# Kernel tuning notes

Hardware: AMD Instinct MI355X
Metric: run time of the kernel (lower is better)

The kernel has to match this reference:

```python
import jax, jax.numpy as jnp
import numpy as np

# Model constants (from Equilibrium3BConfig + hardcoded MambaBlock args)
D_MODEL = 2560
D_INNER = 5120          # expand=2
N_STATE = 128           # d_state
HEADS = 80              # d_inner // headdim
P_HEAD = 64             # headdim
D_CONV = 4
CONV_DIM = D_INNER + 2 * N_STATE        # 5376 (x, B, C share the conv)
D_IN_PROJ = 2 * D_INNER + 2 * N_STATE + HEADS  # 10576 (z, xBC, dt)
N_EXPERTS = 16
TOP_K = 2
M_INTER = 864
MS_INTER = 1728
EPS = 1e-6


def _rms(x, w, eps=EPS):
    xf = x.astype(jnp.float32)
    xf = xf * jax.lax.rsqrt(jnp.mean(xf * xf, axis=-1, keepdims=True) + eps)
    return w * xf.astype(x.dtype)


def setup_inputs() -> dict:
    key = jax.random.key(0)
    ks = jax.random.split(key, 16)
    b, l = 1, 1024
    s = 0.02  # weight scale, keeps activations sane through the deep block
    return {
        "hidden_states": jax.random.normal(ks[0], (b, l, D_MODEL), jnp.float32),
        "w_in": jax.random.normal(ks[1], (D_MODEL, D_IN_PROJ), jnp.float32) * s,
        "conv_w": jax.random.normal(ks[2], (CONV_DIM, D_CONV), jnp.float32) * s,
        "conv_b": jnp.zeros((CONV_DIM,), jnp.float32),
        "dt_bias": jax.random.normal(ks[3], (HEADS,), jnp.float32) * s,
        "A_log": jax.random.normal(ks[4], (HEADS,), jnp.float32) * s,
        "D": jnp.ones((HEADS,), jnp.float32),
        "mamba_norm_w": jnp.ones((D_INNER,), jnp.float32),
        "w_out": jax.random.normal(ks[5], (D_INNER, D_MODEL), jnp.float32) * s,
        "ln1_w": jnp.ones((D_MODEL,), jnp.float32),
        "ln2_w": jnp.ones((D_MODEL,), jnp.float32),
        "router_w": jax.random.normal(ks[6], (D_MODEL, N_EXPERTS), jnp.float32) * s,
        "we_gate": jax.random.normal(ks[7], (N_EXPERTS, D_MODEL, M_INTER), jnp.float32) * s,
        "we_up": jax.random.normal(ks[8], (N_EXPERTS, D_MODEL, M_INTER), jnp.float32) * s,
        "we_down": jax.random.normal(ks[9], (N_EXPERTS, M_INTER, D_MODEL), jnp.float32) * s,
        "ws_gate": jax.random.normal(ks[10], (D_MODEL, MS_INTER), jnp.float32) * s,
        "ws_up": jax.random.normal(ks[11], (D_MODEL, MS_INTER), jnp.float32) * s,
        "ws_down": jax.random.normal(ks[12], (MS_INTER, D_MODEL), jnp.float32) * s,
    }


def _forward(hidden_states, w_in, conv_w, conv_b, dt_bias, A_log, D, mamba_norm_w,
             w_out, ln1_w, ln2_w, router_w, we_gate, we_up, we_down,
             ws_gate, ws_up, ws_down):
    b, l, d = hidden_states.shape

    # ---- Mamba2 (selective scan) sub-block ----
    residual = hidden_states
    x = _rms(hidden_states, ln1_w)
    zxbcdt = x @ w_in  # [b, l, 10576]
    z, xBC, dt = jnp.split(zxbcdt, [D_INNER, D_INNER + CONV_DIM], axis=-1)

    # depthwise causal conv over (x, B, C) channels, then SiLU
    xBC_t = xBC.transpose(0, 2, 1)  # [b, c, l]
    conv = jax.lax.conv_general_dilated(
        xBC_t, conv_w[:, None, :], (1,), [(D_CONV - 1, 0)],
        feature_group_count=CONV_DIM, dimension_numbers=("NCH", "OIH", "NCH"))
    xBC = jax.nn.silu((conv + conv_b[None, :, None]).transpose(0, 2, 1))
    xs, Bc, Cc = jnp.split(xBC, [D_INNER, D_INNER + N_STATE], axis=-1)

    dt = jax.nn.softplus(dt + dt_bias)          # [b, l, h]
    A = -jnp.exp(A_log)                          # [h]
    xh = xs.reshape(b, l, HEADS, P_HEAD)

    # time-major for scan
    dt_l = dt.transpose(1, 0, 2)                 # [l, b, h]
    xh_l = xh.transpose(1, 0, 2, 3)              # [l, b, h, p]
    B_l = Bc.transpose(1, 0, 2)                  # [l, b, n]
    C_l = Cc.transpose(1, 0, 2)                  # [l, b, n]

    def step(h, inp):
        dt_t, x_t, B_t, C_t = inp
        dA = jnp.exp(dt_t * A)                   # [b, h]
        h = h * dA[..., None, None] + (dt_t[..., None] * x_t)[..., None] * B_t[:, None, None, :]
        y = jnp.einsum("bhpn,bn->bhp", h, C_t)
        return h, y

    h0 = jnp.zeros((b, HEADS, P_HEAD, N_STATE), hidden_states.dtype)
    _, y_l = jax.lax.scan(step, h0, (dt_l, xh_l, B_l, C_l))
    y_l = y_l + D[None, None, :, None] * xh_l    # skip term
    y = y_l.transpose(1, 0, 2, 3).reshape(b, l, D_INNER)
    y = _rms(y * jax.nn.silu(z), mamba_norm_w)   # gated RMSNorm
    hidden = residual + y @ w_out

    # ---- DeepSeekMoE sub-block ----
    residual2 = hidden
    xm = _rms(hidden, ln2_w).reshape(b * l, d)
    logits = xm @ router_w
    probs = jax.nn.softmax(logits.astype(jnp.float32), axis=-1)
    topv, topi = jax.lax.top_k(probs, TOP_K)
    topv = topv / jnp.sum(topv, axis=-1, keepdims=True)  # renormalize top-k
    wdense = jnp.sum(jax.nn.one_hot(topi, N_EXPERTS, dtype=xm.dtype)
                     * topv[..., None].astype(xm.dtype), axis=1)  # [T, E]

    # routed experts (SwiGLU), dense-masked faithful math
    hexp = (jax.nn.silu(jnp.einsum("td,edm->tem", xm, we_gate))
            * jnp.einsum("td,edm->tem", xm, we_up))
    y_routed = jnp.einsum("tem,emd,te->td", hexp, we_down, wdense)

    # shared experts (single fused SwiGLU MLP)
    y_shared = (jax.nn.silu(xm @ ws_gate) * (xm @ ws_up)) @ ws_down

    moe = (y_routed + y_shared).reshape(b, l, d)
    return residual2 + moe


def reference(hidden_states, w_in, conv_w, conv_b, dt_bias, A_log, D, mamba_norm_w,
              w_out, ln1_w, ln2_w, router_w, we_gate, we_up, we_down,
              ws_gate, ws_up, ws_down):
    return _forward(hidden_states, w_in, conv_w, conv_b, dt_bias, A_log, D,
                    mamba_norm_w, w_out, ln1_w, ln2_w, router_w,
                    we_gate, we_up, we_down, ws_gate, ws_up, ws_down)
```

## Files before the change

### kernel.cpp

```cpp
#include <hip/hip_runtime.h>

typedef __attribute__((ext_vector_type(4))) float f32x4;
typedef __attribute__((ext_vector_type(8))) __bf16 bf16x8;
typedef __attribute__((ext_vector_type(4))) __bf16 bf16x4;
typedef __attribute__((ext_vector_type(8))) _Float16 f16x8;
typedef __attribute__((ext_vector_type(4))) _Float16 f16x4;

#define D_MODEL 2560
#define D_INNER 5120
#define N_STATE 128
#define HEADS 80
#define P_HEAD 64
#define CONV_DIM 5376
#define D_INPROJ 10576
#define SEQ 1024
#define NCHUNK 16
#define QCHUNK 64
#define NEXP 16
#define M_INTER 864
#define MS_INTER 1728
#define NSLOT 2048
#define NSLOTP 2176

__device__ __forceinline__ float siluf(float x) { return x / (1.f + __expf(-x)); }

__device__ __forceinline__ int swz_p(int k4, int P) {
  return (k4 & ~31) | ((((k4 >> 3) & 3) ^ P) << 3) | (k4 & 7);
}
__device__ __forceinline__ int swz64(int k4, int row) {
  return (k4 & ~63) | (((((k4 >> 3) & 7) ^ (row & 7)) << 3)) | (k4 & 7);
}

__device__ __forceinline__ void gl16(const __bf16* g, __bf16* l) {
  __builtin_amdgcn_global_load_lds((const __attribute__((address_space(1))) unsigned int*)g,
                                   (__attribute__((address_space(3))) unsigned int*)l, 16, 0, 0);
}

__device__ __forceinline__ float block_sum256(float v, float* red) {
#pragma unroll
  for (int m = 32; m > 0; m >>= 1) v += __shfl_xor(v, m, 64);
  int w = threadIdx.x >> 6;
  if ((threadIdx.x & 63) == 0) red[w] = v;
  __syncthreads();
  return red[0] + red[1] + red[2] + red[3];
}

template <bool FP16>
__global__ __launch_bounds__(256) void k_rmsnorm_p(const float* __restrict__ in,
                                                   const float* __restrict__ w,
                                                   float* __restrict__ f32out,
                                                   __bf16* __restrict__ ph,
                                                   __bf16* __restrict__ pdh,
                                                   __bf16* __restrict__ pdl, int D) {
  __shared__ float red[4];
  int t = blockIdx.x, tid = threadIdx.x;
  const float* x = in + (size_t)t * D;
  int nd4 = D >> 2;
  float ss = 0.f;
  for (int i = tid; i < nd4; i += 256) {
    float4 v = ((const float4*)x)[i];
    ss += v.x * v.x + v.y * v.y + v.z * v.z + v.w * v.w;
  }
  float tot = block_sum256(ss, red);
  float r = rsqrtf(tot / (float)D + 1e-6f);
  int P = (t >> 1) & 3;
  for (int i = tid; i < nd4; i += 256) {
    float4 v = ((const float4*)x)[i];
    float4 wv = ((const float4*)w)[i];
    float4 o;
    o.x = wv.x * v.x * r; o.y = wv.y * v.y * r; o.z = wv.z * v.z * r; o.w = wv.w * v.w * r;
    if (f32out) ((float4*)(f32out + (size_t)t * D))[i] = o;
    int p64 = swz64(i * 4, t);
    if constexpr (FP16) {
      f16x4 hv;
      hv[0] = (_Float16)o.x; hv[1] = (_Float16)o.y; hv[2] = (_Float16)o.z; hv[3] = (_Float16)o.w;
      *(f16x4*)&ph[(size_t)t * D + p64] = hv;
    } else {
      bf16x4 hv;
      hv[0] = (__bf16)o.x; hv[1] = (__bf16)o.y; hv[2] = (__bf16)o.z; hv[3] = (__bf16)o.w;
      *(bf16x4*)&ph[(size_t)t * D + p64] = hv;
    }
    if (pdh) {
      int p = swz_p(i * 4, P);
      bf16x4 hv, lv;
      hv[0] = (__bf16)o.x; hv[1] = (__bf16)o.y; hv[2] = (__bf16)o.z; hv[3] = (__bf16)o.w;
      lv[0] = (__bf16)(o.x - (float)hv[0]); lv[1] = (__bf16)(o.y - (float)hv[1]);
      lv[2] = (__bf16)(o.z - (float)hv[2]); lv[3] = (__bf16)(o.w - (float)hv[3]);
      *(bf16x4*)&pdh[(size_t)t * D + p] = hv;
      *(bf16x4*)&pdl[(size_t)t * D + p] = lv;
    }
  }
}

template <bool SPLIT, bool FP16>
__global__ __launch_bounds__(256) void k_transW(const float* __restrict__ W, int ld, int K, int N,
                                                __bf16* __restrict__ Th, __bf16* __restrict__ Tl) {
  __shared__ float T[64][65];
  const int n0 = blockIdx.x * 64, k0 = blockIdx.y * 64, tid = threadIdx.x;
#pragma unroll
  for (int i = 0; i < 16; i++) {
    int idx = tid + i * 256;
    int k = idx >> 6, n = idx & 63;
    float v = 0.f;
    if (n0 + n < N) v = W[(size_t)(k0 + k) * ld + n0 + n];
    T[k][n] = v;
  }
  __syncthreads();
#pragma unroll
  for (int i = 0; i < 4; i++) {
    int idx = tid + i * 256;
    int n = idx >> 4, p4 = (idx & 15) * 4;
    int nn = n0 + n;
    if constexpr (SPLIT) {
      int P = (nn >> 1) & 3;
      bf16x4 hv, lv;
#pragma unroll
      for (int e = 0; e < 4; e++) {
        int p = p4 + e;
        int kk = (p & ~31) | ((((p >> 3) & 3) ^ P) << 3) | (p & 7);
        float v = T[kk][n];
        __bf16 h = (__bf16)v;
        hv[e] = h;
        lv[e] = (__bf16)(v - (float)h);
      }
      *(bf16x4*)&Th[(size_t)nn * K + k0 + p4] = hv;
      *(bf16x4*)&Tl[(size_t)nn * K + k0 + p4] = lv;
    } else if constexpr (FP16) {
      f16x4 hv;
#pragma unroll
      for (int e = 0; e < 4; e++) {
        int p = p4 + e;
        int kk = swz64(p, nn);
        hv[e] = (_Float16)T[kk][n];
      }
      *(f16x4*)&Th[(size_t)nn * K + k0 + p4] = hv;
    } else {
      bf16x4 hv;
#pragma unroll
      for (int e = 0; e < 4; e++) {
        int p = p4 + e;
        int kk = swz64(p, nn);
        hv[e] = (__bf16)T[kk][n];
      }
      *(bf16x4*)&Th[(size_t)nn * K + k0 + p4] = hv;
    }
  }
}

template <bool SPLIT, bool FP16, int BK, bool PIPE>
__global__ __launch_bounds__(256) void k_gemm2(const __bf16* __restrict__ Ah,
                                               const __bf16* __restrict__ Al,
                                               const __bf16* __restrict__ Bh,
                                               const __bf16* __restrict__ Bl,
                                               float* __restrict__ C,
                                               int M, int N, int K, int ks, int nst) {
  constexpr int PLE = 128 * BK;
  constexpr int NPL = SPLIT ? 4 : 2;
  constexpr int NBUF = PIPE ? 2 : 1;
  constexpr int CALLS = PLE / 2048;
  constexpr int CPR = BK / 8;
  constexpr int RPC = 256 / CPR;
  constexpr int KSUB = BK / 32;
  __shared__ __bf16 lds[NBUF * NPL * PLE];

  const int tid = threadIdx.x;
  const int T = gridDim.x * gridDim.y * gridDim.z;
  const int linear = blockIdx.x + gridDim.x * (blockIdx.y + gridDim.y * blockIdx.z);
  const int s_idx = (linear & 7) * (T >> 3) + (linear >> 3);
  const int bm = s_idx & 7;
  const int g = s_idx >> 3;
  const int bn = g % gridDim.y;
  const int z = g / gridDim.y;

  const int m0 = bm * 128, n0 = bn * 128;
  const int s0 = (int)(((long long)z * nst) / ks);
  const int s1 = (int)(((long long)(z + 1) * nst) / ks);
  float* __restrict__ Cp = C + (size_t)z * M * N;

  const int lane = tid & 63, wid = tid >> 6;
  const int wr = wid >> 1, wc = wid & 1;
  const int l16 = lane & 15, kl = lane >> 4;

  const int srow = tid / CPR;
  const int schunk = (tid % CPR) * 8;
  size_t aB[CALLS], bB[CALLS];
#pragma unroll
  for (int i = 0; i < CALLS; i++) {
    aB[i] = (size_t)(m0 + srow + RPC * i) * K + schunk;
    bB[i] = (size_t)(n0 + srow + RPC * i) * K + schunk;
  }

  int aoff[4][KSUB], boff[4][KSUB];
#pragma unroll
  for (int mi = 0; mi < 4; mi++) {
    int ra = wr * 64 + mi * 16 + l16;
    int rb = wc * 64 + mi * 16 + l16;
#pragma unroll
    for (int kk = 0; kk < KSUB; kk++) {
      if constexpr (BK == 32) {
        aoff[mi][kk] = ra * 64 + ((kl ^ ((ra >> 1) & 3)) << 4);
        boff[mi][kk] = rb * 64 + ((kl ^ ((rb >> 1) & 3)) << 4);
      } else {
        aoff[mi][kk] = ra * (2 * BK) + (((kk * 4 + kl) ^ (ra & 7)) << 4);
        boff[mi][kk] = rb * (2 * BK) + (((kk * 4 + kl) ^ (rb & 7)) << 4);
      }
    }
  }

  f32x4 acc[4][4];
#pragma unroll
  for (int mi = 0; mi < 4; mi++)
#pragma unroll
    for (int ni = 0; ni < 4; ni++) acc[mi][ni] = f32x4{0.f, 0.f, 0.f, 0.f};

  auto STAGE = [&](int b, int kof) {
    __bf16* L = lds + (size_t)b * NPL * PLE;
#pragma unroll
    for (int i = 0; i < CALLS; i++) {
      gl16(Ah + aB[i] + kof, L + (tid + i * 256) * 8);
      gl16(Bh + bB[i] + kof, L + (SPLIT ? 2 : 1) * PLE + (tid + i * 256) * 8);
      if constexpr (SPLIT) {
        gl16(Al + aB[i] + kof, L + PLE + (tid + i * 256) * 8);
        gl16(Bl + bB[i] + kof, L + 3 * PLE + (tid + i * 256) * 8);
      }
    }
  };

  auto COMPUTE = [&](const __bf16* L) {
    const char* AsH = (const char*)L;
    const char* BsH = (const char*)(L + (SPLIT ? 2 : 1) * PLE);
#pragma unroll
    for (int kk = 0; kk < KSUB; kk++) {
      if constexpr (!SPLIT && FP16) {
        f16x8 ah[4], bh[4];
#pragma unroll
        for (int mi = 0; mi < 4; mi++) ah[mi] = *(const f16x8*)(AsH + aoff[mi][kk]);
#pragma unroll
        for (int ni = 0; ni < 4; ni++) bh[ni] = *(const f16x8*)(BsH + boff[ni][kk]);
#pragma unroll
        for (int mi = 0; mi < 4; mi++)
#pragma unroll
          for (int ni = 0; ni < 4; ni++)
            acc[mi][ni] = __builtin_amdgcn_mfma_f32_16x16x32_f16(ah[mi], bh[ni], acc[mi][ni], 0, 0, 0);
      } else {
        bf16x8 ah[4], bh[4];
#pragma unroll
        for (int mi = 0; mi < 4; mi++) ah[mi] = *(const bf16x8*)(AsH + aoff[mi][kk]);
#pragma unroll
        for (int ni = 0; ni < 4; ni++) bh[ni] = *(const bf16x8*)(BsH + boff[ni][kk]);
#pragma unroll
        for (int mi = 0; mi < 4; mi++)
#pragma unroll
          for (int ni = 0; ni < 4; ni++)
            acc[mi][ni] = __builtin_amdgcn_mfma_f32_16x16x32_bf16(ah[mi], bh[ni], acc[mi][ni], 0, 0, 0);
        if constexpr (SPLIT) {
          const char* AsL = (const char*)(L + PLE);
          const char* BsL = (const char*)(L + 3 * PLE);
          bf16x8 al[4], bl[4];
#pragma unroll
          for (int mi = 0; mi < 4; mi++) al[mi] = *(const bf16x8*)(AsL + aoff[mi][kk]);
#pragma unroll
          for (int ni = 0; ni < 4; ni++) bl[ni] = *(const bf16x8*)(BsL + boff[ni][kk]);
#pragma unroll
          for (int mi = 0; mi < 4; mi++)
#pragma unroll
            for (int ni = 0; ni < 4; ni++) {
              acc[mi][ni] = __builtin_amdgcn_mfma_f32_16x16x32_bf16(ah[mi], bl[ni], acc[mi][ni], 0, 0, 0);
              acc[mi][ni] = __builtin_amdgcn_mfma_f32_16x16x32_bf16(al[mi], bh[ni], acc[mi][ni], 0, 0, 0);
            }
        }
      }
    }
  };

  if constexpr (PIPE) {
    STAGE(0, s0 * BK);
    __syncthreads();
    int cur = 0;
    for (int s = s0; s < s1; ++s) {
      if (s + 1 < s1) STAGE(cur ^ 1, (s + 1) * BK);
      COMPUTE(lds + (size_t)cur * NPL * PLE);
      __syncthreads();
      cur ^= 1;
    }
  } else {
    for (int s = s0; s < s1; ++s) {
      __syncthreads();
      STAGE(0, s * BK);
      __syncthreads();
      COMPUTE(lds);
    }
  }

#pragma unroll
  for (int mi = 0; mi < 4; mi++)
#pragma unroll
    for (int ni = 0; ni < 4; ni++)
#pragma unroll
      for (int r = 0; r < 4; r++) {
        int row = m0 + wr * 64 + mi * 16 + kl * 4 + r;
        int col = n0 + wc * 64 + ni * 16 + l16;
        if (col < N) Cp[(size_t)row * N + col] = acc[mi][ni][r];
      }
}

template <bool RES>
__global__ void k_reduce(const float* __restrict__ Pp, int np, int n4,
                         const float* __restrict__ res, float* __restrict__ out) {
  int i = blockIdx.x * 256 + threadIdx.x;
  int stride = gridDim.x * 256;
  for (; i < n4; i += stride) {
    float4 a = ((const float4*)Pp)[i];
    for (int z = 1; z < np; z++) {
      float4 b = ((const float4*)Pp)[(size_t)z * n4 + i];
      a.x += b.x; a.y += b.y; a.z += b.z; a.w += b.w;
    }
    if constexpr (RES) {
      float4 r0 = ((const float4*)res)[i];
      a.x += r0.x; a.y += r0.y; a.z += r0.z; a.w += r0.w;
    }
    ((float4*)out)[i] = a;
  }
}

__global__ void k_dtfin(const float* __restrict__ dtP, const float* __restrict__ dt_bias,
                        const float* __restrict__ A_log, float* __restrict__ dtp,
                        float* __restrict__ dtA) {
  int t = blockIdx.x, h = threadIdx.x;
  if (h < HEADS) {
    float v = dt_bias[h];
#pragma unroll
    for (int z = 0; z < 8; z++) v += dtP[((size_t)z * SEQ + t) * 80 + h];
    float sp = fmaxf(v, 0.f) + log1pf(expf(-fabsf(v)));
    dtp[t * HEADS + h] = sp;
    dtA[t * HEADS + h] = sp * (-expf(A_log[h]));
  }
}

__global__ __launch_bounds__(256) void k_gatherA(const float* __restrict__ xm,
                                                 const int* __restrict__ perm,
                                                 __bf16* __restrict__ Aslots) {
  int s = blockIdx.x, tid = threadIdx.x;
  int t = perm[s];
  int P = (s >> 1) & 3;
  const float* src = xm + (size_t)t * D_MODEL;
  __bf16* dst = Aslots + (size_t)s * D_MODEL;
  for (int i = tid; i < D_MODEL / 4; i += 256) {
    float4 v = ((const float4*)src)[i];
    int p = swz_p(i * 4, P);
    bf16x4 h;
    h[0] = (__bf16)v.x; h[1] = (__bf16)v.y; h[2] = (__bf16)v.z; h[3] = (__bf16)v.w;
    *(bf16x4*)&dst[p] = h;
  }
}

template <int KS>
__global__ __launch_bounds__(256) void k_gemmE2(const __bf16* __restrict__ Aall,
                                                const float* __restrict__ Bg,
                                                float* __restrict__ Cp,
                                                const int* __restrict__ expOff,
                                                const int* __restrict__ expCnt,
                                                int N, int K, long long strideB) {
  __shared__ __bf16 Asl[2][128 * 32];
  __shared__ __bf16 Bsl[2][128][40];
  const int tid = threadIdx.x;
  const int bn = blockIdx.x, ks = blockIdx.y, e = blockIdx.z;
  const int cnt = expCnt[e], base = expOff[e];
  if (cnt == 0) return;
  const float* Bp = Bg + (long long)e * strideB;
  const int n0 = bn * 128;
  const int kChunk = K / KS, kBeg = ks * kChunk, nIter = kChunk / 32;
  float* __restrict__ Cpl = Cp + (size_t)ks * NSLOTP * N;
  const int lane = tid & 63, wid = tid >> 6;
  const int wr = wid >> 1, wc = wid & 1;
  const int l16 = lane & 15, kl = lane >> 4;
  const int kb = tid >> 5, cb = tid & 31;
  const int arow = tid >> 2, achk = (tid & 3) * 8;
  const bool bok = (n0 + cb * 4) < N;

  int boffs[4];
#pragma unroll
  for (int ni = 0; ni < 4; ni++) boffs[ni] = (wc * 64 + ni * 16 + l16) * 40 + kl * 8;

  for (int bm = 0; bm * 128 < cnt; ++bm) {
    const int rbase = base + bm * 128;
    int aoff[4];
#pragma unroll
    for (int mi = 0; mi < 4; mi++) {
      int r = wr * 64 + mi * 16 + l16;
      int P = ((rbase + r) >> 1) & 3;
      aoff[mi] = r * 64 + ((kl ^ P) << 4);
    }
    f32x4 acc[4][4];
#pragma unroll
    for (int mi = 0; mi < 4; mi++)
#pragma unroll
      for (int ni = 0; ni < 4; ni++) acc[mi][ni] = f32x4{0.f, 0.f, 0.f, 0.f};

    const size_t aBase = (size_t)(rbase + arow) * K + achk + kBeg;
    const size_t aBase2 = aBase + (size_t)64 * K;

    gl16(Aall + aBase, &Asl[0][tid * 8]);
    gl16(Aall + aBase2, &Asl[0][(tid + 256) * 8]);
    {
      const float* src = Bp + (size_t)(kBeg + kb * 4) * N + n0 + cb * 4;
      f32x4 bv[4];
#pragma unroll
      for (int j = 0; j < 4; j++)
        bv[j] = bok ? *(const f32x4*)(src + (size_t)j * N) : f32x4{0.f, 0.f, 0.f, 0.f};
#pragma unroll
      for (int e4 = 0; e4 < 4; e4++) {
        bf16x4 h;
        h[0] = (__bf16)bv[0][e4]; h[1] = (__bf16)bv[1][e4];
        h[2] = (__bf16)bv[2][e4]; h[3] = (__bf16)bv[3][e4];
        *(bf16x4*)&Bsl[0][cb * 4 + e4][kb * 4] = h;
      }
    }
    __syncthreads();
    int cur = 0;
    for (int kt = 0; kt < nIter; ++kt) {
      const bool more = (kt + 1 < nIter);
      f32x4 nv[4];
      if (more) {
        const int kOff = (kt + 1) * 32;
        gl16(Aall + aBase + kOff, &Asl[cur ^ 1][tid * 8]);
// ... 16 lines not shown
      if (more) {
#pragma unroll
        for (int e4 = 0; e4 < 4; e4++) {
          bf16x4 h;
          h[0] = (__bf16)nv[0][e4]; h[1] = (__bf16)nv[1][e4];
          h[2] = (__bf16)nv[2][e4]; h[3] = (__bf16)nv[3][e4];
          *(bf16x4*)&Bsl[cur ^ 1][cb * 4 + e4][kb * 4] = h;
        }
      }
      __syncthreads();
      cur ^= 1;
    }
#pragma unroll
    for (int mi = 0; mi < 4; mi++)
#pragma unroll
      for (int ni = 0; ni < 4; ni++)
#pragma unroll
        for (int r = 0; r < 4; r++) {
          int rl = bm * 128 + wr * 64 + mi * 16 + kl * 4 + r;
          int col = n0 + wc * 64 + ni * 16 + l16;
          if (rl < cnt && col < N) Cpl[(size_t)(base + rl) * N + col] = acc[mi][ni][r];
        }
  }
}

__global__ __launch_bounds__(256) void k_silumulE(const float* __restrict__ gP,
                                                  const float* __restrict__ uP,
                                                  const float* __restrict__ slotw,
                                                  __bf16* __restrict__ outp) {
  int s = blockIdx.x, tid = threadIdx.x;
  float w = slotw[s];
  int P = (s >> 1) & 3;
  const size_t PL = (size_t)NSLOTP * M_INTER;
  for (int i = tid; i < M_INTER / 4; i += 256) {
    f32x4 g = f32x4{0.f, 0.f, 0.f, 0.f}, u = f32x4{0.f, 0.f, 0.f, 0.f};
#pragma unroll
    for (int z = 0; z < 4; z++) {
      g += *(const f32x4*)&gP[z * PL + (size_t)s * M_INTER + i * 4];
      u += *(const f32x4*)&uP[z * PL + (size_t)s * M_INTER + i * 4];
    }
    int p = swz_p(i * 4, P);
    bf16x4 h;
    h[0] = (__bf16)(siluf(g[0]) * u[0] * w);
    h[1] = (__bf16)(siluf(g[1]) * u[1] * w);
    h[2] = (__bf16)(siluf(g[2]) * u[2] * w);
    h[3] = (__bf16)(siluf(g[3]) * u[3] * w);
    *(bf16x4*)&outp[(size_t)s * M_INTER + p] = h;
  }
}

__global__ __launch_bounds__(256) void k_silumul_sh2(const float* __restrict__ P4,
                                                     __bf16* __restrict__ outp) {
  int t = blockIdx.x, tid = threadIdx.x;
  const size_t PL = (size_t)SEQ * 3456;
  for (int i = tid; i < MS_INTER / 4; i += 256) {
    f32x4 g = f32x4{0.f, 0.f, 0.f, 0.f}, u = f32x4{0.f, 0.f, 0.f, 0.f};
#pragma unroll
    for (int z = 0; z < 4; z++) {
      g += *(const f32x4*)&P4[z * PL + (size_t)t * 3456 + i * 4];
      u += *(const f32x4*)&P4[z * PL + (size_t)t * 3456 + 1728 + i * 4];
    }
    int p = swz64(i * 4, t);
    bf16x4 h;
    h[0] = (__bf16)(siluf(g[0]) * u[0]);
    h[1] = (__bf16)(siluf(g[1]) * u[1]);
    h[2] = (__bf16)(siluf(g[2]) * u[2]);
    h[3] = (__bf16)(siluf(g[3]) * u[3]);
    *(bf16x4*)&outp[(size_t)t * MS_INTER + p] = h;
  }
}

__global__ void k_conv(const float* __restrict__ zx, const float* __restrict__ cw,
                       const float* __restrict__ cb, float* __restrict__ xBC) {
  int cidx = blockIdx.x * 256 + threadIdx.x;
  int t = blockIdx.y;
  if (cidx < CONV_DIM) {
    float acc = cb[cidx];
#pragma unroll
    for (int j = 0; j < 4; j++) {
      int tt = t - 3 + j;
      if (tt >= 0) acc += zx[(size_t)tt * D_INPROJ + D_INNER + cidx] * cw[cidx * 4 + j];
    }
    xBC[(size_t)t * CONV_DIM + cidx] = siluf(acc);
  }
}

__global__ __launch_bounds__(256) void k_scan_intra(
    const float* __restrict__ xBC, const float* __restrict__ dtp,
    const float* __restrict__ dtA, float* __restrict__ y, float* __restrict__ S,
    float* __restrict__ cumA, float* __restrict__ Atot) {
  __shared__ float Bs[64 * 128];
  __shared__ float CG[64 * 128];
  __shared__ _Float16 Xs[64 * 64];
  __shared__ float da_s[64], a_s[64], dt_sh[64], w_sh[64];
  int c = blockIdx.x, h = blockIdx.y, tid = threadIdx.x;
  int t0 = c * QCHUNK;
#pragma unroll
  for (int i = 0; i < 8; i++) {
    int id = tid + 256 * i;
    int r = id >> 5, nc = id & 31;
    int sc = (nc ^ ((r >> 2) & 7)) * 4;
    *(float4*)&Bs[r * 128 + sc] = *(const float4*)&xBC[(size_t)(t0 + r) * CONV_DIM + D_INNER + nc * 4];
    *(float4*)&CG[r * 128 + sc] = *(const float4*)&xBC[(size_t)(t0 + r) * CONV_DIM + D_INNER + N_STATE + nc * 4];
  }
#pragma unroll
  for (int i = 0; i < 4; i++) {
    int id = tid + 256 * i;
    int r = id >> 4, p4 = (id & 15) * 4;
    float4 v = *(const float4*)&xBC[(size_t)(t0 + r) * CONV_DIM + h * P_HEAD + p4];
    f16x4 hv;
    hv[0] = (_Float16)v.x; hv[1] = (_Float16)v.y; hv[2] = (_Float16)v.z; hv[3] = (_Float16)v.w;
    *(f16x4*)&Xs[r * 64 + p4] = hv;
  }
  if (tid < 64) {
    da_s[tid] = dtA[(size_t)(t0 + tid) * HEADS + h];
// ... 133 lines not shown
#pragma unroll
  for (int j = 0; j < 4; j++) acc[j] = float4{0.f, 0.f, 0.f, 0.f};
  for (int nc = 0; nc < 32; nc++) {
    float4 cv[4], hv[4];
#pragma unroll
    for (int j = 0; j < 4; j++) {
      int rt = tq * 4 + j;
      cv[j] = *(const float4*)&Cs[rt * 128 + ((nc ^ ((rt >> 2) & 7)) * 4)];
      int rp = pq * 4 + j;
      hv[j] = *(const float4*)&Hs[rp * 128 + ((nc ^ ((rp >> 2) & 7)) * 4)];
    }
#pragma unroll
    for (int j = 0; j < 4; j++) {
      acc[j].x += cv[j].x * hv[0].x + cv[j].y * hv[0].y + cv[j].z * hv[0].z + cv[j].w * hv[0].w;
      acc[j].y += cv[j].x * hv[1].x + cv[j].y * hv[1].y + cv[j].z * hv[1].z + cv[j].w * hv[1].w;
      acc[j].z += cv[j].x * hv[2].x + cv[j].y * hv[2].y + cv[j].z * hv[2].z + cv[j].w * hv[2].w;
      acc[j].w += cv[j].x * hv[3].x + cv[j].y * hv[3].y + cv[j].z * hv[3].z + cv[j].w * hv[3].w;
    }
  }
#pragma unroll
  for (int j = 0; j < 4; j++) {
    int t = tq * 4 + j;
    float e = __expf(a_l[t]);
    float4 xv = *(const float4*)&xBC[(size_t)(t0 + t) * CONV_DIM + h * P_HEAD + pq * 4];
    size_t yoff = (size_t)(t0 + t) * D_INNER + h * P_HEAD + pq * 4;
    float4 yv = *(float4*)&y[yoff];
    yv.x += e * acc[j].x + Dh * xv.x;
    yv.y += e * acc[j].y + Dh * xv.y;
    yv.z += e * acc[j].z + Dh * xv.z;
    yv.w += e * acc[j].w + Dh * xv.w;
    *(float4*)&y[yoff] = yv;
  }
}

__global__ __launch_bounds__(256) void k_gatednorm_p(const float* __restrict__ y,
                                                     const float* __restrict__ zx,
                                                     const float* __restrict__ w,
                                                     __bf16* __restrict__ ph) {
  __shared__ float vbuf[D_INNER];
  __shared__ float red[4];
  int t = blockIdx.x, tid = threadIdx.x;
  float ss = 0.f;
  for (int i = tid; i < D_INNER / 4; i += 256) {
    float4 yv = *(const float4*)&y[(size_t)t * D_INNER + i * 4];
    float4 zv = *(const float4*)&zx[(size_t)t * D_INPROJ + i * 4];
    float4 v;
    v.x = yv.x * siluf(zv.x); v.y = yv.y * siluf(zv.y);
    v.z = yv.z * siluf(zv.z); v.w = yv.w * siluf(zv.w);
    *(float4*)&vbuf[i * 4] = v;
    ss += v.x * v.x + v.y * v.y + v.z * v.z + v.w * v.w;
  }
  float tot = block_sum256(ss, red);
  float r = rsqrtf(tot / (float)D_INNER + 1e-6f);
  for (int i = tid; i < D_INNER / 4; i += 256) {
    float4 v = *(const float4*)&vbuf[i * 4];
    float4 wv = *(const float4*)&w[i * 4];
    float4 o;
    o.x = wv.x * v.x * r; o.y = wv.y * v.y * r; o.z = wv.z * v.z * r; o.w = wv.w * v.w * r;
    int p = swz64(i * 4, t);
    f16x4 hv;
    hv[0] = (_Float16)o.x; hv[1] = (_Float16)o.y; hv[2] = (_Float16)o.z; hv[3] = (_Float16)o.w;
    *(f16x4*)&ph[(size_t)t * D_INNER + p] = hv;
  }
}

__global__ void k_zero(int* counts, int* cursor) {
  int i = threadIdx.x;
  if (i < NEXP) { counts[i] = 0; cursor[i] = 0; }
}

__global__ __launch_bounds__(256) void k_router(const float* __restrict__ xm,
                                                const float* __restrict__ Wr,
                                                int* __restrict__ top_i,
                                                float* __restrict__ top_v,
                                                int* __restrict__ counts) {
  __shared__ float part[16][17];
  __shared__ float lg[16];
  int t = blockIdx.x, tid = threadIdx.x;
  int e = tid & 15, seg = tid >> 4;
  const float* xr = xm + (size_t)t * D_MODEL;
  float s = 0.f;
  for (int i = 0; i < 160; i++) {
    int k = seg * 160 + i;
    s += xr[k] * Wr[(size_t)k * NEXP + e];
  }
  part[seg][e] = s;
  __syncthreads();
  if (tid < 16) {
    float l = 0.f;
    for (int g = 0; g < 16; g++) l += part[g][tid];
    lg[tid] = l;
  }
  __syncthreads();
  if (tid == 0) {
    float mx = lg[0];
    for (int i = 1; i < 16; i++) mx = fmaxf(mx, lg[i]);
    float pe[16];
    for (int i = 0; i < 16; i++) pe[i] = expf(lg[i] - mx);
    int i0 = 0; float v0 = pe[0];
    for (int i = 1; i < 16; i++) if (pe[i] > v0) { v0 = pe[i]; i0 = i; }
    int i1 = -1; float v1 = -1.f;
    for (int i = 0; i < 16; i++) if (i != i0 && pe[i] > v1) { v1 = pe[i]; i1 = i; }
    float inv = 1.f / (v0 + v1);
    top_i[t * 2] = i0; top_i[t * 2 + 1] = i1;
    top_v[t * 2] = v0 * inv; top_v[t * 2 + 1] = v1 * inv;
    atomicAdd(&counts[i0], 1);
    atomicAdd(&counts[i1], 1);
  }
}

__global__ void k_offsets(const int* counts, int* offs, int* cursor) {
  if (threadIdx.x == 0) {
// ... 62 lines not shown
  char* base = (char*)d_ws;
  size_t off = 0;
  auto A = [&](size_t bytes) -> void* {
    void* p = base + off;
    off += (bytes + 255) & ~(size_t)255;
    return p;
  };
  float* xbc = (float*)A((size_t)SEQ * CONV_DIM * 4);
  float* xmf = (float*)A((size_t)SEQ * D_MODEL * 4);
  float* dtp = (float*)A((size_t)SEQ * HEADS * 4);
  float* dtA = (float*)A((size_t)SEQ * HEADS * 4);
  float* yf = (float*)A((size_t)SEQ * D_INNER * 4);
  float* cumA = (float*)A((size_t)NCHUNK * HEADS * QCHUNK * 4);
  float* Atot = (float*)A((size_t)NCHUNK * HEADS * 4);
  float* Sbuf = (float*)A((size_t)NCHUNK * HEADS * 64 * 128 * 4);
  float* hidden = (float*)A((size_t)SEQ * D_MODEL * 4);
  float* shout = (float*)A((size_t)SEQ * D_MODEL * 4);
  float* top_v = (float*)A(8192);
  float* slotw = (float*)A(8192);
  int* top_i = (int*)A(8192);
  int* counts = (int*)A(64);
  int* offs = (int*)A(64);
  int* cursor = (int*)A(64);
  int* perm = (int*)A(8192);
  int* slotOf = (int*)A(8192);
  __bf16* xp_h = (__bf16*)A((size_t)SEQ * D_MODEL * 2);
  __bf16* ybp_h = (__bf16*)A((size_t)SEQ * D_INNER * 2);
  __bf16* gbuf_bh = (__bf16*)A((size_t)SEQ * MS_INTER * 2);
  char* REG = (char*)A((size_t)163000000);

  __bf16* winT_h = (__bf16*)REG;
  float* zx = (float*)(REG + 60000000);
  float* partials = (float*)(REG + 104000000);
  __bf16* xdt_h = (__bf16*)(REG + 147000000);
  __bf16* xdt_l = (__bf16*)(REG + 152500000);
  __bf16* wdt_h = (__bf16*)(REG + 158000000);
  __bf16* wdt_l = (__bf16*)(REG + 158700000);
  float* dtP = (float*)(REG + 159400000);
  __bf16* woutT_h = (__bf16*)REG;
  __bf16* guT = (__bf16*)REG;
  __bf16* downT = (__bf16*)(REG + 18350080);
  float* partials4 = (float*)(REG + 30000000);
  __bf16* Aslots = (__bf16*)REG;
  __bf16* gsl = (__bf16*)(REG + 12000000);
  float* gateP = (float*)(REG + 16000000);
  float* upP = (float*)(REG + 47000000);
  float* dslotsP = (float*)(REG + 78000000);

  k_rmsnorm_p<true><<<SEQ, 256, 0, stream>>>(hs, ln1, nullptr, xp_h, xdt_h, xdt_l, D_MODEL);
  k_transW<false, true><<<dim3(166, 40), 256, 0, stream>>>(w_in, D_INPROJ, D_MODEL, D_INPROJ,
                                                           winT_h, nullptr);
  k_transW<true, false><<<dim3(2, 40), 256, 0, stream>>>(w_in + 10496, D_INPROJ, D_MODEL, 80,
                                                         wdt_h, wdt_l);
  k_gemm2<false, true, 64, true><<<dim3(8, 83, 1), 256, 0, stream>>>(
      xp_h, nullptr, winT_h, nullptr, zx, SEQ, D_INPROJ, D_MODEL, 1, 40);
  k_gemm2<true, false, 32, false><<<dim3(8, 1, 8), 256, 0, stream>>>(
      xdt_h, xdt_l, wdt_h, wdt_l, dtP, SEQ, 80, D_MODEL, 8, 80);
  k_dtfin<<<SEQ, 128, 0, stream>>>(dtP, dt_bias, A_log, dtp, dtA);
  k_conv<<<dim3(21, SEQ), 256, 0, stream>>>(zx, conv_w, conv_b, xbc);
  k_scan_intra<<<dim3(NCHUNK, HEADS), 256, 0, stream>>>(xbc, dtp, dtA, yf, Sbuf, cumA, Atot);
  k_scan_state<<<2560, 256, 0, stream>>>(Sbuf, Atot);
  k_scan_inter<<<dim3(NCHUNK, HEADS), 256, 0, stream>>>(xbc, Sbuf, cumA, Dv, yf);
  k_gatednorm_p<<<SEQ, 256, 0, stream>>>(yf, zx, mnw, ybp_h);
  k_transW<false, true><<<dim3(40, 80), 256, 0, stream>>>(w_out, D_MODEL, D_INNER, D_MODEL,
                                                          woutT_h, nullptr);
  k_gemm2<false, true, 64, true><<<dim3(8, 20, 4), 256, 0, stream>>>(
      ybp_h, nullptr, woutT_h, nullptr, partials, SEQ, D_MODEL, D_INNER, 4, 80);
  k_reduce<true><<<2048, 256, 0, stream>>>(partials, 4, SEQ * D_MODEL / 4, hs, hidden);

  k_rmsnorm_p<false><<<SEQ, 256, 0, stream>>>(hidden, ln2, xmf, xp_h, nullptr, nullptr, D_MODEL);
  k_zero<<<1, 64, 0, stream>>>(counts, cursor);
  k_router<<<SEQ, 256, 0, stream>>>(xmf, router_w, top_i, top_v, counts);
  k_offsets<<<1, 32, 0, stream>>>(counts, offs, cursor);
  k_scatter<<<4, 256, 0, stream>>>(top_i, top_v, cursor, perm, slotOf, slotw);

  k_transW<false, false><<<dim3(27, 40), 256, 0, stream>>>(ws_gate, MS_INTER, D_MODEL, MS_INTER,
                                                           guT, nullptr);
  k_transW<false, false><<<dim3(27, 40), 256, 0, stream>>>(ws_up, MS_INTER, D_MODEL, MS_INTER,
                                                           guT + (size_t)MS_INTER * D_MODEL, nullptr);
  k_gemm2<false, false, 64, true><<<dim3(8, 27, 4), 256, 0, stream>>>(
      xp_h, nullptr, guT, nullptr, partials4, SEQ, 3456, D_MODEL, 4, 40);
  k_silumul_sh2<<<SEQ, 256, 0, stream>>>(partials4, gbuf_bh);
  k_transW<false, false><<<dim3(40, 27), 256, 0, stream>>>(ws_down, D_MODEL, MS_INTER, D_MODEL,
                                                           downT, nullptr);
  k_gemm2<false, false, 64, true><<<dim3(8, 20, 4), 256, 0, stream>>>(
      gbuf_bh, nullptr, downT, nullptr, partials4, SEQ, D_MODEL, MS_INTER, 4, 27);
  k_reduce<false><<<2048, 256, 0, stream>>>(partials4, 4, SEQ * D_MODEL / 4, nullptr, shout);

  k_gatherA<<<NSLOT, 256, 0, stream>>>(xmf, perm, Aslots);
  k_gemmE2<4><<<dim3(7, 4, NEXP), 256, 0, stream>>>(Aslots, we_gate, gateP, offs, counts,
                                                    M_INTER, D_MODEL, (long long)D_MODEL * M_INTER);
  k_gemmE2<4><<<dim3(7, 4, NEXP), 256, 0, stream>>>(Aslots, we_up, upP, offs, counts,
                                                    M_INTER, D_MODEL, (long long)D_MODEL * M_INTER);
  k_silumulE<<<NSLOT, 256, 0, stream>>>(gateP, upP, slotw, gsl);
  k_gemmE2<3><<<dim3(20, 3, NEXP), 256, 0, stream>>>(gsl, we_down, dslotsP, offs, counts,
                                                     D_MODEL, M_INTER, (long long)M_INTER * D_MODEL);

  k_final2<<<dim3(3, SEQ), 256, 0, stream>>>(hidden, shout, dslotsP, slotOf, (float*)d_out);
}
```

Measured before the change: 791.0 us.

## Fuse reduce with RMSNorm, merge expert gate/up GEMMs, revert GEMM to BK=32

Adds k_redrms, which sums the split-K partials of the out-projection, adds the residual and applies the second RMSNorm in a single kernel, replacing a reduce pass and a norm pass. The routed expert gate and up projections now run as one dual-output launch, selected by block index, instead of two launches. The dense GEMM template drops its BK parameter and always uses a 32-wide K step with a 4-row XOR swizzle. Every producer of GEMM inputs moves to that swizzle, and the stage counts double to match. The smaller K step halves the work per pipeline iteration, so each block does twice as many barriers and stage loads.

```diff
diff --git a/kernel.cpp b/kernel.cpp
--- a/kernel.cpp
+++ b/kernel.cpp
@@ -27,9 +27,6 @@
 __device__ __forceinline__ int swz_p(int k4, int P) {
   return (k4 & ~31) | ((((k4 >> 3) & 3) ^ P) << 3) | (k4 & 7);
 }
-__device__ __forceinline__ int swz64(int k4, int row) {
-  return (k4 & ~63) | (((((k4 >> 3) & 7) ^ (row & 7)) << 3)) | (k4 & 7);
-}
 
 __device__ __forceinline__ void gl16(const __bf16* g, __bf16* l) {
   __builtin_amdgcn_global_load_lds((const __attribute__((address_space(1))) unsigned int*)g,
@@ -70,25 +67,61 @@
     float4 o;
     o.x = wv.x * v.x * r; o.y = wv.y * v.y * r; o.z = wv.z * v.z * r; o.w = wv.w * v.w * r;
     if (f32out) ((float4*)(f32out + (size_t)t * D))[i] = o;
-    int p64 = swz64(i * 4, t);
+    int p = swz_p(i * 4, P);
     if constexpr (FP16) {
       f16x4 hv;
       hv[0] = (_Float16)o.x; hv[1] = (_Float16)o.y; hv[2] = (_Float16)o.z; hv[3] = (_Float16)o.w;
-      *(f16x4*)&ph[(size_t)t * D + p64] = hv;
+      *(f16x4*)&ph[(size_t)t * D + p] = hv;
     } else {
       bf16x4 hv;
       hv[0] = (__bf16)o.x; hv[1] = (__bf16)o.y; hv[2] = (__bf16)o.z; hv[3] = (__bf16)o.w;
-      *(bf16x4*)&ph[(size_t)t * D + p64] = hv;
+      *(bf16x4*)&ph[(size_t)t * D + p] = hv;
     }
     if (pdh) {
-      int p = swz_p(i * 4, P);
+      int pp = swz_p(i * 4, P);
       bf16x4 hv, lv;
       hv[0] = (__bf16)o.x; hv[1] = (__bf16)o.y; hv[2] = (__bf16)o.z; hv[3] = (__bf16)o.w;
       lv[0] = (__bf16)(o.x - (float)hv[0]); lv[1] = (__bf16)(o.y - (float)hv[1]);
       lv[2] = (__bf16)(o.z - (float)hv[2]); lv[3] = (__bf16)(o.w - (float)hv[3]);
-      *(bf16x4*)&pdh[(size_t)t * D + p] = hv;
-      *(bf16x4*)&pdl[(size_t)t * D + p] = lv;
-    }
+      *(bf16x4*)&pdh[(size_t)t * D + pp] = hv;
+      *(bf16x4*)&pdl[(size_t)t * D + pp] = lv;
+    }
+  }
+}
+
+__global__ __launch_bounds__(256) void k_redrms(const float* __restrict__ Pp,
+                                                const float* __restrict__ res,
+                                                float* __restrict__ hidden,
+                                                const float* __restrict__ w,
+                                                float* __restrict__ f32out,
+                                                __bf16* __restrict__ ph) {
+  __shared__ float vbuf[D_MODEL];
+  __shared__ float red[4];
+  int t = blockIdx.x, tid = threadIdx.x;
+  const int n4 = D_MODEL / 4;
+  float ss = 0.f;
+  for (int i = tid; i < n4; i += 256) {
+    f32x4 a = *(const f32x4*)&res[(size_t)t * D_MODEL + i * 4];
+#pragma unroll
+    for (int z = 0; z < 4; z++)
+      a += *(const f32x4*)&Pp[(size_t)z * SEQ * D_MODEL + (size_t)t * D_MODEL + i * 4];
+    *(f32x4*)&vbuf[i * 4] = a;
+    *(f32x4*)&hidden[(size_t)t * D_MODEL + i * 4] = a;
+    ss += a[0] * a[0] + a[1] * a[1] + a[2] * a[2] + a[3] * a[3];
+  }
+  float tot = block_sum256(ss, red);
+  float r = rsqrtf(tot / (float)D_MODEL + 1e-6f);
+  int P = (t >> 1) & 3;
+  for (int i = tid; i < n4; i += 256) {
+    f32x4 v = *(const f32x4*)&vbuf[i * 4];
+    float4 wv = *(const float4*)&w[i * 4];
+    f32x4 o;
+    o[0] = wv.x * v[0] * r; o[1] = wv.y * v[1] * r; o[2] = wv.z * v[2] * r; o[3] = wv.w * v[3] * r;
+    *(f32x4*)&f32out[(size_t)t * D_MODEL + i * 4] = o;
+    int p = swz_p(i * 4, P);
+    bf16x4 hv;
+    hv[0] = (__bf16)o[0]; hv[1] = (__bf16)o[1]; hv[2] = (__bf16)o[2]; hv[3] = (__bf16)o[3];
+    *(bf16x4*)&ph[(size_t)t * D_MODEL + p] = hv;
   }
 }
 
@@ -111,13 +144,13 @@
     int idx = tid + i * 256;
     int n = idx >> 4, p4 = (idx & 15) * 4;
     int nn = n0 + n;
+    int P = (nn >> 1) & 3;
     if constexpr (SPLIT) {
-      int P = (nn >> 1) & 3;
       bf16x4 hv, lv;
 #pragma unroll
       for (int e = 0; e < 4; e++) {
         int p = p4 + e;
-        int kk = (p & ~31) | ((((p >> 3) & 3) ^ P) << 3) | (p & 7);
+        int kk = swz_p(p, P);
         float v = T[kk][n];
         __bf16 h = (__bf16)v;
         hv[e] = h;
@@ -130,7 +163,7 @@
 #pragma unroll
       for (int e = 0; e < 4; e++) {
         int p = p4 + e;
-        int kk = swz64(p, nn);
+        int kk = swz_p(p, P);
         hv[e] = (_Float16)T[kk][n];
       }
       *(f16x4*)&Th[(size_t)nn * K + k0 + p4] = hv;
@@ -139,7 +172,7 @@
 #pragma unroll
       for (int e = 0; e < 4; e++) {
         int p = p4 + e;
-        int kk = swz64(p, nn);
+        int kk = swz_p(p, P);
         hv[e] = (__bf16)T[kk][n];
       }
       *(bf16x4*)&Th[(size_t)nn * K + k0 + p4] = hv;
@@ -147,20 +180,16 @@
   }
 }
 
-template <bool SPLIT, bool FP16, int BK, bool PIPE>
+template <bool SPLIT, bool FP16, bool PIPE>
 __global__ __launch_bounds__(256) void k_gemm2(const __bf16* __restrict__ Ah,
                                                const __bf16* __restrict__ Al,
                                                const __bf16* __restrict__ Bh,
                                                const __bf16* __restrict__ Bl,
                                                float* __restrict__ C,
                                                int M, int N, int K, int ks, int nst) {
-  constexpr int PLE = 128 * BK;
+  constexpr int PLE = 4096;
   constexpr int NPL = SPLIT ? 4 : 2;
   constexpr int NBUF = PIPE ? 2 : 1;
-  constexpr int CALLS = PLE / 2048;
-  constexpr int CPR = BK / 8;
-  constexpr int RPC = 256 / CPR;
-  constexpr int KSUB = BK / 32;
   __shared__ __bf16 lds[NBUF * NPL * PLE];
 
   const int tid = threadIdx.x;
@@ -181,30 +210,20 @@
   const int wr = wid >> 1, wc = wid & 1;
   const int l16 = lane & 15, kl = lane >> 4;
 
-  const int srow = tid / CPR;
-  const int schunk = (tid % CPR) * 8;
-  size_t aB[CALLS], bB[CALLS];
-#pragma unroll
-  for (int i = 0; i < CALLS; i++) {
-    aB[i] = (size_t)(m0 + srow + RPC * i) * K + schunk;
-    bB[i] = (size_t)(n0 + srow + RPC * i) * K + schunk;
-  }
-
-  int aoff[4][KSUB], boff[4][KSUB];
+  const int srow = tid >> 2;
+  const int schunk = (tid & 3) * 8;
+  const size_t aB0 = (size_t)(m0 + srow) * K + schunk;
+  const size_t aB1 = aB0 + (size_t)64 * K;
+  const size_t bB0 = (size_t)(n0 + srow) * K + schunk;
+  const size_t bB1 = bB0 + (size_t)64 * K;
+
+  int aoff[4], boff[4];
 #pragma unroll
   for (int mi = 0; mi < 4; mi++) {
     int ra = wr * 64 + mi * 16 + l16;
     int rb = wc * 64 + mi * 16 + l16;
-#pragma unroll
-    for (int kk = 0; kk < KSUB; kk++) {
-      if constexpr (BK == 32) {
-        aoff[mi][kk] = ra * 64 + ((kl ^ ((ra >> 1) & 3)) << 4);
-        boff[mi][kk] = rb * 64 + ((kl ^ ((rb >> 1) & 3)) << 4);
-      } else {
-        aoff[mi][kk] = ra * (2 * BK) + (((kk * 4 + kl) ^ (ra & 7)) << 4);
-        boff[mi][kk] = rb * (2 * BK) + (((kk * 4 + kl) ^ (rb & 7)) << 4);
-      }
-    }
+    aoff[mi] = ra * 64 + ((kl ^ ((ra >> 1) & 3)) << 4);
+    boff[mi] = rb * 64 + ((kl ^ ((rb >> 1) & 3)) << 4);
   }
 
   f32x4 acc[4][4];
@@ -215,70 +234,68 @@
 
   auto STAGE = [&](int b, int kof) {
     __bf16* L = lds + (size_t)b * NPL * PLE;
-#pragma unroll
-    for (int i = 0; i < CALLS; i++) {
-      gl16(Ah + aB[i] + kof, L + (tid + i * 256) * 8);
-      gl16(Bh + bB[i] + kof, L + (SPLIT ? 2 : 1) * PLE + (tid + i * 256) * 8);
-      if constexpr (SPLIT) {
-        gl16(Al + aB[i] + kof, L + PLE + (tid + i * 256) * 8);
-        gl16(Bl + bB[i] + kof, L + 3 * PLE + (tid + i * 256) * 8);
-      }
+    gl16(Ah + aB0 + kof, L + tid * 8);
+    gl16(Ah + aB1 + kof, L + (tid + 256) * 8);
+    gl16(Bh + bB0 + kof, L + (SPLIT ? 2 : 1) * PLE + tid * 8);
+    gl16(Bh + bB1 + kof, L + (SPLIT ? 2 : 1) * PLE + (tid + 256) * 8);
+    if constexpr (SPLIT) {
+      gl16(Al + aB0 + kof, L + PLE + tid * 8);
+      gl16(Al + aB1 + kof, L + PLE + (tid + 256) * 8);
+      gl16(Bl + bB0 + kof, L + 3 * PLE + tid * 8);
+      gl16(Bl + bB1 + kof, L + 3 * PLE + (tid + 256) * 8);
     }
   };
 
   auto COMPUTE = [&](const __bf16* L) {
     const char* AsH = (const char*)L;
     const char* BsH = (const char*)(L + (SPLIT ? 2 : 1) * PLE);
-#pragma unroll
-    for (int kk = 0; kk < KSUB; kk++) {
-      if constexpr (!SPLIT && FP16) {
-        f16x8 ah[4], bh[4];
-#pragma unroll
-        for (int mi = 0; mi < 4; mi++) ah[mi] = *(const f16x8*)(AsH + aoff[mi][kk]);
-#pragma unroll
-        for (int ni = 0; ni < 4; ni++) bh[ni] = *(const f16x8*)(BsH + boff[ni][kk]);
+    if constexpr (!SPLIT && FP16) {
+      f16x8 ah[4], bh[4];
+#pragma unroll
+      for (int mi = 0; mi < 4; mi++) ah[mi] = *(const f16x8*)(AsH + aoff[mi]);
+#pragma unroll
+      for (int ni = 0; ni < 4; ni++) bh[ni] = *(const f16x8*)(BsH + boff[ni]);
+#pragma unroll
+      for (int mi = 0; mi < 4; mi++)
+#pragma unroll
+        for (int ni = 0; ni < 4; ni++)
+          acc[mi][ni] = __builtin_amdgcn_mfma_f32_16x16x32_f16(ah[mi], bh[ni], acc[mi][ni], 0, 0, 0);
+    } else {
+      bf16x8 ah[4], bh[4];
+#pragma unroll
+      for (int mi = 0; mi < 4; mi++) ah[mi] = *(const bf16x8*)(AsH + aoff[mi]);
+#pragma unroll
+      for (int ni = 0; ni < 4; ni++) bh[ni] = *(const bf16x8*)(BsH + boff[ni]);
+#pragma unroll
+      for (int mi = 0; mi < 4; mi++)
+#pragma unroll
+        for (int ni = 0; ni < 4; ni++)
+          acc[mi][ni] = __builtin_amdgcn_mfma_f32_16x16x32_bf16(ah[mi], bh[ni], acc[mi][ni], 0, 0, 0);
+      if constexpr (SPLIT) {
+        const char* AsL = (const char*)(L + PLE);
+        const char* BsL = (const char*)(L + 3 * PLE);
+        bf16x8 al[4], bl[4];
+#pragma unroll
+        for (int mi = 0; mi < 4; mi++) al[mi] = *(const bf16x8*)(AsL + aoff[mi]);
+#pragma unroll
+        for (int ni = 0; ni < 4; ni++) bl[ni] = *(const bf16x8*)(BsL + boff[ni]);
 #pragma unroll
         for (int mi = 0; mi < 4; mi++)
 #pragma unroll
-          for (int ni = 0; ni < 4; ni++)
-            acc[mi][ni] = __builtin_amdgcn_mfma_f32_16x16x32_f16(ah[mi], bh[ni], acc[mi][ni], 0, 0, 0);
-      } else {
-        bf16x8 ah[4], bh[4];
-#pragma unroll
-        for (int mi = 0; mi < 4; mi++) ah[mi] = *(const bf16x8*)(AsH + aoff[mi][kk]);
-#pragma unroll
-        for (int ni = 0; ni < 4; ni++) bh[ni] = *(const bf16x8*)(BsH + boff[ni][kk]);
-#pragma unroll
-        for (int mi = 0; mi < 4; mi++)
-#pragma unroll
-          for (int ni = 0; ni < 4; ni++)
-            acc[mi][ni] = __builtin_amdgcn_mfma_f32_16x16x32_bf16(ah[mi], bh[ni], acc[mi][ni], 0, 0, 0);
-        if constexpr (SPLIT) {
-          const char* AsL = (const char*)(L + PLE);
-          const char* BsL = (const char*)(L + 3 * PLE);
-          bf16x8 al[4], bl[4];
-#pragma unroll
-          for (int mi = 0; mi < 4; mi++) al[mi] = *(const bf16x8*)(AsL + aoff[mi][kk]);
-#pragma unroll
-          for (int ni = 0; ni < 4; ni++) bl[ni] = *(const bf16x8*)(BsL + boff[ni][kk]);
-#pragma unroll
-          for (int mi = 0; mi < 4; mi++)
-#pragma unroll
-            for (int ni = 0; ni < 4; ni++) {
-              acc[mi][ni] = __builtin_amdgcn_mfma_f32_16x16x32_bf16(ah[mi], bl[ni], acc[mi][ni], 0, 0, 0);
-              acc[mi][ni] = __builtin_amdgcn_mfma_f32_16x16x32_bf16(al[mi], bh[ni], acc[mi][ni], 0, 0, 0);
-            }
-        }
+          for (int ni = 0; ni < 4; ni++) {
+            acc[mi][ni] = __builtin_amdgcn_mfma_f32_16x16x32_bf16(ah[mi], bl[ni], acc[mi][ni], 0, 0, 0);
+            acc[mi][ni] = __builtin_amdgcn_mfma_f32_16x16x32_bf16(al[mi], bh[ni], acc[mi][ni], 0, 0, 0);
+          }
       }
     }
   };
 
   if constexpr (PIPE) {
-    STAGE(0, s0 * BK);
+    STAGE(0, s0 * 32);
     __syncthreads();
     int cur = 0;
     for (int s = s0; s < s1; ++s) {
-      if (s + 1 < s1) STAGE(cur ^ 1, (s + 1) * BK);
+      if (s + 1 < s1) STAGE(cur ^ 1, (s + 1) * 32);
       COMPUTE(lds + (size_t)cur * NPL * PLE);
       __syncthreads();
       cur ^= 1;
@@ -286,7 +303,7 @@
   } else {
     for (int s = s0; s < s1; ++s) {
       __syncthreads();
-      STAGE(0, s * BK);
+      STAGE(0, s * 32);
       __syncthreads();
       COMPUTE(lds);
     }
@@ -304,9 +321,7 @@
       }
 }
 
-template <bool RES>
-__global__ void k_reduce(const float* __restrict__ Pp, int np, int n4,
-                         const float* __restrict__ res, float* __restrict__ out) {
+__global__ void k_reduce(const float* __restrict__ Pp, int np, int n4, float* __restrict__ out) {
   int i = blockIdx.x * 256 + threadIdx.x;
   int stride = gridDim.x * 256;
   for (; i < n4; i += stride) {
@@ -314,10 +329,6 @@
     for (int z = 1; z < np; z++) {
       float4 b = ((const float4*)Pp)[(size_t)z * n4 + i];
       a.x += b.x; a.y += b.y; a.z += b.z; a.w += b.w;
-    }
-    if constexpr (RES) {
-      float4 r0 = ((const float4*)res)[i];
-      a.x += r0.x; a.y += r0.y; a.z += r0.z; a.w += r0.w;
     }
     ((float4*)out)[i] = a;
   }
@@ -354,23 +365,35 @@
   }
 }
 
-template <int KS>
+template <int KS, bool DUAL>
 __global__ __launch_bounds__(256) void k_gemmE2(const __bf16* __restrict__ Aall,
                                                 const float* __restrict__ Bg,
+                                                const float* __restrict__ Bg2,
                                                 float* __restrict__ Cp,
+                                                float* __restrict__ Cp2,
                                                 const int* __restrict__ expOff,
                                                 const int* __restrict__ expCnt,
-                                                int N, int K, long long strideB) {
+                                                int N, int K, long long strideB, int bnHalf) {
   __shared__ __bf16 Asl[2][128 * 32];
   __shared__ __bf16 Bsl[2][128][40];
   const int tid = threadIdx.x;
-  const int bn = blockIdx.x, ks = blockIdx.y, e = blockIdx.z;
+  int bn = blockIdx.x;
+  const int ks = blockIdx.y, e = blockIdx.z;
   const int cnt = expCnt[e], base = expOff[e];
   if (cnt == 0) return;
-  const float* Bp = Bg + (long long)e * strideB;
+  const float* Bp = Bg;
+  float* Cdst = Cp;
+  if constexpr (DUAL) {
+    if (bn >= bnHalf) {
+      bn -= bnHalf;
+      Bp = Bg2;
+      Cdst = Cp2;
+    }
+  }
+  Bp += (long long)e * strideB;
   const int n0 = bn * 128;
   const int kChunk = K / KS, kBeg = ks * kChunk, nIter = kChunk / 32;
-  float* __restrict__ Cpl = Cp + (size_t)ks * NSLOTP * N;
+  float* __restrict__ Cpl = Cdst + (size_t)ks * NSLOTP * N;
   const int lane = tid & 63, wid = tid >> 6;
   const int wr = wid >> 1, wc = wid & 1;
   const int l16 = lane & 15, kl = lane >> 4;
@@ -493,6 +516,7 @@
 __global__ __launch_bounds__(256) void k_silumul_sh2(const float* __restrict__ P4,
                                                      __bf16* __restrict__ outp) {
   int t = blockIdx.x, tid = threadIdx.x;
+  int P = (t >> 1) & 3;
   const size_t PL = (size_t)SEQ * 3456;
   for (int i = tid; i < MS_INTER / 4; i += 256) {
     f32x4 g = f32x4{0.f, 0.f, 0.f, 0.f}, u = f32x4{0.f, 0.f, 0.f, 0.f};
@@ -501,7 +525,7 @@
       g += *(const f32x4*)&P4[z * PL + (size_t)t * 3456 + i * 4];
       u += *(const f32x4*)&P4[z * PL + (size_t)t * 3456 + 1728 + i * 4];
     }
-    int p = swz64(i * 4, t);
+    int p = swz_p(i * 4, P);
     bf16x4 h;
     h[0] = (__bf16)(siluf(g[0]) * u[0]);
     h[1] = (__bf16)(siluf(g[1]) * u[1]);
@@ -741,12 +765,13 @@
   }
   float tot = block_sum256(ss, red);
   float r = rsqrtf(tot / (float)D_INNER + 1e-6f);
+  int P = (t >> 1) & 3;
   for (int i = tid; i < D_INNER / 4; i += 256) {
     float4 v = *(const float4*)&vbuf[i * 4];
     float4 wv = *(const float4*)&w[i * 4];
     float4 o;
     o.x = wv.x * v.x * r; o.y = wv.y * v.y * r; o.z = wv.z * v.z * r; o.w = wv.w * v.w * r;
-    int p = swz64(i * 4, t);
+    int p = swz_p(i * 4, P);
     f16x4 hv;
     hv[0] = (_Float16)o.x; hv[1] = (_Float16)o.y; hv[2] = (_Float16)o.z; hv[3] = (_Float16)o.w;
     *(f16x4*)&ph[(size_t)t * D_INNER + p] = hv;
@@ -915,9 +940,9 @@
                                                            winT_h, nullptr);
   k_transW<true, false><<<dim3(2, 40), 256, 0, stream>>>(w_in + 10496, D_INPROJ, D_MODEL, 80,
                                                          wdt_h, wdt_l);
-  k_gemm2<false, true, 64, true><<<dim3(8, 83, 1), 256, 0, stream>>>(
-      xp_h, nullptr, winT_h, nullptr, zx, SEQ, D_INPROJ, D_MODEL, 1, 40);
-  k_gemm2<true, false, 32, false><<<dim3(8, 1, 8), 256, 0, stream>>>(
+  k_gemm2<false, true, true><<<dim3(8, 83, 1), 256, 0, stream>>>(
+      xp_h, nullptr, winT_h, nullptr, zx, SEQ, D_INPROJ, D_MODEL, 1, 80);
+  k_gemm2<true, false, false><<<dim3(8, 1, 8), 256, 0, stream>>>(
       xdt_h, xdt_l, wdt_h, wdt_l, dtP, SEQ, 80, D_MODEL, 8, 80);
   k_dtfin<<<SEQ, 128, 0, stream>>>(dtP, dt_bias, A_log, dtp, dtA);
   k_conv<<<dim3(21, SEQ), 256, 0, stream>>>(zx, conv_w, conv_b, xbc);
@@ -927,11 +952,10 @@
   k_gatednorm_p<<<SEQ, 256, 0, stream>>>(yf, zx, mnw, ybp_h);
   k_transW<false, true><<<dim3(40, 80), 256, 0, stream>>>(w_out, D_MODEL, D_INNER, D_MODEL,
                                                           woutT_h, nullptr);
-  k_gemm2<false, true, 64, true><<<dim3(8, 20, 4), 256, 0, stream>>>(
-      ybp_h, nullptr, woutT_h, nullptr, partials, SEQ, D_MODEL, D_INNER, 4, 80);
-  k_reduce<true><<<2048, 256, 0, stream>>>(partials, 4, SEQ * D_MODEL / 4, hs, hidden);
-
-  k_rmsnorm_p<false><<<SEQ, 256, 0, stream>>>(hidden, ln2, xmf, xp_h, nullptr, nullptr, D_MODEL);
+  k_gemm2<false, true, true><<<dim3(8, 20, 4), 256, 0, stream>>>(
+      ybp_h, nullptr, woutT_h, nullptr, partials, SEQ, D_MODEL, D_INNER, 4, 160);
+  k_redrms<<<SEQ, 256, 0, stream>>>(partials, hs, hidden, ln2, xmf, xp_h);
+
   k_zero<<<1, 64, 0, stream>>>(counts, cursor);
   k_router<<<SEQ, 256, 0, stream>>>(xmf, router_w, top_i, top_v, counts);
   k_offsets<<<1, 32, 0, stream>>>(counts, offs, cursor);
@@ -941,23 +965,23 @@
                                                            guT, nullptr);
   k_transW<false, false><<<dim3(27, 40), 256, 0, stream>>>(ws_up, MS_INTER, D_MODEL, MS_INTER,
                                                            guT + (size_t)MS_INTER * D_MODEL, nullptr);
-  k_gemm2<false, false, 64, true><<<dim3(8, 27, 4), 256, 0, stream>>>(
-      xp_h, nullptr, guT, nullptr, partials4, SEQ, 3456, D_MODEL, 4, 40);
+  k_gemm2<false, false, true><<<dim3(8, 27, 4), 256, 0, stream>>>(
+      xp_h, nullptr, guT, nullptr, partials4, SEQ, 3456, D_MODEL, 4, 80);
   k_silumul_sh2<<<SEQ, 256, 0, stream>>>(partials4, gbuf_bh);
   k_transW<false, false><<<dim3(40, 27), 256, 0, stream>>>(ws_down, D_MODEL, MS_INTER, D_MODEL,
                                                            downT, nullptr);
-  k_gemm2<false, false, 64, true><<<dim3(8, 20, 4), 256, 0, stream>>>(
-      gbuf_bh, nullptr, downT, nullptr, partials4, SEQ, D_MODEL, MS_INTER, 4, 27);
-  k_reduce<false><<<2048, 256, 0, stream>>>(partials4, 4, SEQ * D_MODEL / 4, nullptr, shout);
+  k_gemm2<false, false, true><<<dim3(8, 20, 4), 256, 0, stream>>>(
+      gbuf_bh, nullptr, downT, nullptr, partials4, SEQ, D_MODEL, MS_INTER, 4, 54);
+  k_reduce<<<2048, 256, 0, stream>>>(partials4, 4, SEQ * D_MODEL / 4, shout);
 
   k_gatherA<<<NSLOT, 256, 0, stream>>>(xmf, perm, Aslots);
-  k_gemmE2<4><<<dim3(7, 4, NEXP), 256, 0, stream>>>(Aslots, we_gate, gateP, offs, counts,
-                                                    M_INTER, D_MODEL, (long long)D_MODEL * M_INTER);
-  k_gemmE2<4><<<dim3(7, 4, NEXP), 256, 0, stream>>>(Aslots, we_up, upP, offs, counts,
-                                                    M_INTER, D_MODEL, (long long)D_MODEL * M_INTER);
+  k_gemmE2<4, true><<<dim3(14, 4, NEXP), 256, 0, stream>>>(
+      Aslots, we_gate, we_up, gateP, upP, offs, counts,
+      M_INTER, D_MODEL, (long long)D_MODEL * M_INTER, 7);
   k_silumulE<<<NSLOT, 256, 0, stream>>>(gateP, upP, slotw, gsl);
-  k_gemmE2<3><<<dim3(20, 3, NEXP), 256, 0, stream>>>(gsl, we_down, dslotsP, offs, counts,
-                                                     D_MODEL, M_INTER, (long long)M_INTER * D_MODEL);
+  k_gemmE2<3, false><<<dim3(20, 3, NEXP), 256, 0, stream>>>(
+      gsl, we_down, nullptr, dslotsP, nullptr, offs, counts,
+      D_MODEL, M_INTER, (long long)M_INTER * D_MODEL, 0);
 
   k_final2<<<dim3(3, SEQ), 256, 0, stream>>>(hidden, shout, dslotsP, slotOf, (float*)d_out);
 }
```

Result: faster. 750.0 us (-5.2%).
